# Kernel optimization log

Measured on AMD Instinct MI355X. Metric: run time of the kernel, lower is better.

The kernel has to match this reference:

```python
import jax, jax.numpy as jnp
import numpy as np

B, N, K, H = 8, 256, 64, 768
NUM_CLASSES = 10
D_SIM = 0.3  # self.d in the torch module


def setup_inputs() -> dict:
    key = jax.random.key(0)
    ks = jax.random.split(key, 12)
    s = 0.02  # init scale to keep 3 stacked linear GCN layers numerically tame
    return {
        "encoder_out": jax.random.normal(ks[0], (B, N, H), jnp.float32),
        "landmarks": jax.random.normal(ks[1], (K, H), jnp.float32),
        "alpha": jnp.array([0.5], jnp.float32),
        "gcn_w1": jax.random.normal(ks[2], (H, H), jnp.float32) * s,
        "gcn_b1": jnp.zeros((H,), jnp.float32),
        "gcn_w2": jax.random.normal(ks[3], (H, H), jnp.float32) * s,
        "gcn_b2": jnp.zeros((H,), jnp.float32),
        "gcn_w3": jax.random.normal(ks[4], (H, H), jnp.float32) * s,
        "gcn_b3": jnp.zeros((H,), jnp.float32),
        "fc1_w": jax.random.normal(ks[5], (1000, K * H), jnp.float32) * s,
        "fc1_b": jnp.zeros((1000,), jnp.float32),
        "fc2_w": jax.random.normal(ks[6], (100, 1000), jnp.float32) * s,
        "fc2_b": jnp.zeros((100,), jnp.float32),
        "fc3_w": jax.random.normal(ks[7], (NUM_CLASSES, 100), jnp.float32) * s,
        "fc3_b": jnp.zeros((NUM_CLASSES,), jnp.float32),
    }


def reference(encoder_out, landmarks, alpha,
              gcn_w1, gcn_b1, gcn_w2, gcn_b2, gcn_w3, gcn_b3,
              fc1_w, fc1_b, fc2_w, fc2_b, fc3_w, fc3_b):
    b, n, h = encoder_out.shape
    k = landmarks.shape[0]

    # distance_matrix: [B,N,K], min-max normalized over clusters
    diff = encoder_out[:, :, None, :] - landmarks[None, None, :, :]  # [B,N,K,H]
    dist = jnp.sqrt(jnp.sum(diff * diff, axis=-1))                   # [B,N,K]
    mn = dist.min(axis=-1, keepdims=True)
    mx = dist.max(axis=-1, keepdims=True)
    nd = (dist - mn) / (mx - mn + 1e-6)

    # probability_matrix: gaussian similarity, row-normalized
    sim = jnp.exp(-nd * nd / (2.0 * D_SIM * D_SIM))
    prob = sim / sim.sum(axis=-1, keepdims=True)  # [B,N,K]

    # compute_distance_weight: [N,N] smooth matrix
    idx = jnp.arange(n)
    dw = jnp.exp(-alpha[0] * jnp.abs(idx[:, None] - idx[None, :]).astype(jnp.float32))

    # graph_constructing: einsum('bik,bjl->bijkl') * W then sum over (k,l)
    # == bilinear form P @ W @ P^T, computed WITHOUT the 5-D tensor
    P = prob.transpose(0, 2, 1)                      # [B,K,N]
    G = jnp.einsum('bik,kl,bjl->bij', P, dw, P)      # [B,K,K]

    # cluster pooling: prob^T @ encoder_out -> [B,K,H]
    out = jnp.einsum('bnk,bnh->bkh', prob, encoder_out)
    out_ori = out  # dropout is identity at inference

    # gcn_batched: PyG GCNConv x3 on the dense graph G!=0, batched.
    # gcn_norm: add remaining self-loops, A_hat = A + I_missing,
    # out = D^-1/2 A_hat D^-1/2 (X W^T) + bias  (no nonlinearity between layers)
    A = (G != 0).astype(jnp.float32)                 # [B,K,K]
    A = jnp.maximum(A, jnp.eye(k, dtype=jnp.float32))
    deg = A.sum(axis=-1)                             # [B,K]
    dinv = jnp.where(deg > 0, 1.0 / jnp.sqrt(deg), 0.0)
    An = A * dinv[:, :, None] * dinv[:, None, :]     # normalized adjacency

    hx = out
    for w, bias in ((gcn_w1, gcn_b1), (gcn_w2, gcn_b2), (gcn_w3, gcn_b3)):
        hx = jnp.einsum('bij,bjh->bih', An, hx @ w.T) + bias
    gcn_out = hx + out  # residual inside gcn_batched

    x = (out_ori + gcn_out).reshape(b, -1)           # [B, K*H]
    x = jax.nn.gelu(x @ fc1_w.T + fc1_b, approximate=False)
    x = jax.nn.gelu(x @ fc2_w.T + fc2_b, approximate=False)
    return x @ fc3_w.T + fc3_b                       # [B, NUM_CLASSES]
```

## Files before the change

kernel.cpp:

```cpp
#include <hip/hip_runtime.h>
#include <math.h>

#define DEV __device__ __forceinline__

DEV float dot4(float4 a, float4 b){ return a.x*b.x + a.y*b.y + a.z*b.z + a.w*b.w; }

DEV float wave_sum(float v){
  #pragma unroll
  for (int off = 32; off; off >>= 1) v += __shfl_xor(v, off, 64);
  return v;
}

DEV float gelu_exact(float v){ return 0.5f * v * (1.f + erff(v * 0.70710678118654752f)); }

__global__ void __launch_bounds__(256) k_prob(const float* __restrict__ lm,
                                              const float* __restrict__ enc,
                                              float* __restrict__ prob,
                                              float* __restrict__ y1zero){
  int t = threadIdx.x, lane = t & 63, wv = t >> 6;
  int gid = blockIdx.x*256 + t;
  if (gid < 8000) y1zero[gid] = 0.f;
  int row0 = blockIdx.x*8 + wv*2;
  __shared__ float4 ls[3072];
  const float4* L4 = (const float4*)lm;
  const float4* X0 = (const float4*)(enc + (size_t)row0*768);
  const float4* X1 = X0 + 192;
  float dot0=0.f, dot1=0.f, xn0=0.f, xn1=0.f, ln=0.f;
  for (int c = 0; c < 4; ++c){
    if (c) __syncthreads();
    #pragma unroll
    for (int i = 0; i < 12; ++i){
      int idx = i*256 + t;
      int k = idx & 63, col = idx >> 6;
      ls[idx] = L4[k*192 + c*48 + col];
    }
    __syncthreads();
    #pragma unroll 8
    for (int hg = 0; hg < 48; ++hg){
      float4 l4 = ls[hg*64 + lane];
      float4 a = X0[c*48 + hg], b = X1[c*48 + hg];
      dot0 += dot4(a, l4); dot1 += dot4(b, l4);
      xn0  += dot4(a, a);  xn1  += dot4(b, b);
      ln   += dot4(l4, l4);
    }
  }
  float d0 = sqrtf(fmaxf(xn0 + ln - 2.f*dot0, 0.f));
  float d1 = sqrtf(fmaxf(xn1 + ln - 2.f*dot1, 0.f));
  float mn0=d0, mx0=d0, mn1=d1, mx1=d1;
  #pragma unroll
  for (int off = 32; off; off >>= 1){
    mn0 = fminf(mn0, __shfl_xor(mn0, off, 64));
    mx0 = fmaxf(mx0, __shfl_xor(mx0, off, 64));
    mn1 = fminf(mn1, __shfl_xor(mn1, off, 64));
    mx1 = fmaxf(mx1, __shfl_xor(mx1, off, 64));
  }
  float nd0 = (d0 - mn0) / (mx0 - mn0 + 1e-6f);
  float nd1 = (d1 - mn1) / (mx1 - mn1 + 1e-6f);
  float s0 = expf(nd0*nd0 * (-1.f/0.18f));
  float s1 = expf(nd1*nd1 * (-1.f/0.18f));
  float sum0 = wave_sum(s0), sum1 = wave_sum(s1);
  prob[(size_t)row0*64 + lane]     = s0 / sum0;
  prob[(size_t)(row0+1)*64 + lane] = s1 / sum1;
}

__global__ void k_pool(const float* __restrict__ enc, const float* __restrict__ prob,
                       float* __restrict__ outp, float* __restrict__ mbar){
  int b = blockIdx.x / 48, ch = blockIdx.x % 48;
  int lane = threadIdx.x & 63, wv = threadIdx.x >> 6;
  int h0 = ch*16 + wv*4;
  const float* E = enc + (size_t)b*256*768 + h0;
  const float* P = prob + (size_t)b*256*64;
  float acc[4] = {0,0,0,0};
  #pragma unroll 4
  for (int n = 0; n < 256; ++n){
    float p = P[n*64 + lane];
    float4 e0 = *(const float4*)(E + (size_t)n*768);
    acc[0] += p*e0.x; acc[1] += p*e0.y; acc[2] += p*e0.z; acc[3] += p*e0.w;
  }
  float* O = outp + ((size_t)b*64 + lane)*768 + h0;
  *(float4*)O = make_float4(acc[0],acc[1],acc[2],acc[3]);
  #pragma unroll
  for (int j = 0; j < 4; ++j){
    float v = wave_sum(acc[j]);
    if (lane == 0) mbar[(size_t)b*768 + h0 + j] = v * (1.f/64.f);
  }
}

__global__ void k_vm768(const float* __restrict__ in, const float* __restrict__ W,
                        const float* __restrict__ bias, float* __restrict__ out){
  int lane = threadIdx.x & 63, wv = threadIdx.x >> 6;
  int j = blockIdx.x*4 + wv;
  const float4* Wr = (const float4*)(W + (size_t)j*768);
  const float4* IN = (const float4*)in;
  float acc[8] = {0,0,0,0,0,0,0,0};
  #pragma unroll
  for (int s = 0; s < 3; ++s){
    int ig = s*64 + lane;
    float4 w4 = Wr[ig];
    #pragma unroll
    for (int b = 0; b < 8; ++b) acc[b] += dot4(w4, IN[b*192 + ig]);
  }
  #pragma unroll
  for (int b = 0; b < 8; ++b){
    float v = wave_sum(acc[b]);
    if (lane == 0) out[b*768 + j] = v + bias[j];
  }
}

__global__ void __launch_bounds__(256) k_fc1s(const float* __restrict__ outp,
                                              const float* __restrict__ hx3,
                                              const float* __restrict__ W,
                                              float* __restrict__ y1){
  int t = threadIdx.x, lane = t & 63, wv = t >> 6;
  int kc = blockIdx.x / 125, jg = blockIdx.x % 125;
  int j0 = jg*8;
  const float4* O4 = (const float4*)outp + kc*384;
  const float4* H4 = (const float4*)hx3;
  const float4* Wa = (const float4*)W + (size_t)(j0 + wv*2)*12288 + kc*384;
  const float4* Wb = Wa + 12288;
  __shared__ float4 xs4[3072];
  __shared__ float sp[64];

  float4 wa[6], wb[6];
  #pragma unroll
  for (int s = 0; s < 6; ++s){ wa[s] = Wa[s*64 + lane]; wb[s] = Wb[s*64 + lane]; }

  #pragma unroll
  for (int i = 0; i < 12; ++i){
    int idx = i*256 + t;
    int b = idx / 384, r = idx - b*384;
    int hf4 = r - (r >= 192 ? 192 : 0);
    float4 o = O4[(size_t)b*12288 + r];
    float4 g = H4[b*192 + hf4];
    float4 v;
    v.x = 2.f*o.x + g.x; v.y = 2.f*o.y + g.y; v.z = 2.f*o.z + g.z; v.w = 2.f*o.w + g.w;
    xs4[idx] = v;
  }
  __syncthreads();

  float acc0[8] = {0,0,0,0,0,0,0,0};
  float acc1[8] = {0,0,0,0,0,0,0,0};
  #pragma unroll
  for (int s = 0; s < 6; ++s){
    int ig = s*64 + lane;
    #pragma unroll
    for (int b = 0; b < 8; ++b){
      float4 xv = xs4[b*384 + ig];
      acc0[b] += dot4(wa[s], xv);
      acc1[b] += dot4(wb[s], xv);
    }
  }

  #pragma unroll
  for (int b = 0; b < 8; ++b){
    float v0 = wave_sum(acc0[b]);
    float v1 = wave_sum(acc1[b]);
    if (lane == 0){ sp[(wv*2+0)*8 + b] = v0; sp[(wv*2+1)*8 + b] = v1; }
  }
  __syncthreads();
  if (t < 64){
    int jp = t >> 3, b = t & 7;
    atomicAdd(&y1[b*1000 + j0 + jp], sp[t]);
  }
}

__global__ void __launch_bounds__(256) k_tail(const float* __restrict__ y1,
                                              const float* __restrict__ fb1,
                                              const float* __restrict__ W2,
                                              const float* __restrict__ fb2,
                                              const float* __restrict__ W3,
                                              const float* __restrict__ fb3,
                                              float* __restrict__ out){
  int b = blockIdx.x, t = threadIdx.x, lane = t & 63, wv = t >> 6;
  __shared__ __align__(16) float x1s[1000];
  __shared__ float x2s[100];
  #pragma unroll
  for (int i = 0; i < 4; ++i){
    int j = i*256 + t;
    if (j < 1000) x1s[j] = gelu_exact(y1[b*1000 + j] + fb1[j]);
  }
  __syncthreads();
  const float4* X4 = (const float4*)x1s;
  for (int i = 0; i < 25; ++i){
    int m = wv*25 + i;
    const float4* Wr = (const float4*)(W2 + (size_t)m*1000);
    float acc = 0.f;
    #pragma unroll
    for (int s = 0; s < 4; ++s){
      int jg = s*64 + lane;
      if (jg < 250) acc += dot4(Wr[jg], X4[jg]);
    }
    acc = wave_sum(acc);
    if (lane == 0) x2s[m] = gelu_exact(acc + fb2[m]);
  }
  __syncthreads();
  if (t < 10){
    float acc = fb3[t];
    const float* Wr = W3 + t*100;
    #pragma unroll 4
    for (int m = 0; m < 100; ++m) acc += x2s[m]*Wr[m];
    out[b*10 + t] = acc;
  }
}

extern "C" void kernel_launch(void* const* d_in, const int* in_sizes, int n_in,
                              void* d_out, int out_size, void* d_ws, size_t ws_size,
                              hipStream_t stream){
  const float* enc = (const float*)d_in[0];
  const float* lm  = (const float*)d_in[1];
  const float* w1  = (const float*)d_in[3];
  const float* b1  = (const float*)d_in[4];
  const float* w2  = (const float*)d_in[5];
  const float* b2  = (const float*)d_in[6];
  const float* w3  = (const float*)d_in[7];
  const float* b3  = (const float*)d_in[8];
  const float* fw1 = (const float*)d_in[9];
  const float* fb1 = (const float*)d_in[10];
  const float* fw2 = (const float*)d_in[11];
  const float* fb2 = (const float*)d_in[12];
  const float* fw3 = (const float*)d_in[13];
  const float* fb3 = (const float*)d_in[14];

  float* ws    = (float*)d_ws;
  float* prob  = ws;
  float* outp  = prob  + 131072;
  float* mbar  = outp  + 393216;
  float* hx1   = mbar  + 6144;
  float* hx2   = hx1   + 6144;
  float* hx3   = hx2   + 6144;
  float* y1raw = hx3   + 6144;
  float* out   = (float*)d_out;

  k_prob <<<256, 256, 0, stream>>>(lm, enc, prob, y1raw);
  k_pool <<<384, 256, 0, stream>>>(enc, prob, outp, mbar);
  k_vm768<<<192, 256, 0, stream>>>(mbar, w1, b1, hx1);
  k_vm768<<<192, 256, 0, stream>>>(hx1,  w2, b2, hx2);
  k_vm768<<<192, 256, 0, stream>>>(hx2,  w3, b3, hx3);
  k_fc1s <<<4000,256, 0, stream>>>(outp, hx3, fw1, y1raw);
  k_tail <<<8,   256, 0, stream>>>(y1raw, fb1, fw2, fb2, fw3, fb3, out);
}
```

Measured before the change: 159.2 us.

## Restructure fc1 split-K: 4 rows per wave, partial buffers instead of atomics

The fc1 kernel now gives each wave 4 output rows instead of 2, halving the block count. It reads the activation directly from global/L2 instead of staging it through shared memory, which removes the block barriers. Per-chunk partial sums go to a [32,1000,8] buffer that the tail kernel reduces, replacing the atomicAdd path and the zeroing in k_prob. The trade-offs are more registers per thread (24 float4 weights plus 32 accumulators), repeated global reads of the activation, and a 32-way serial reduction in the tail.

```diff
diff --git a/kernel.cpp b/kernel.cpp
--- a/kernel.cpp
+++ b/kernel.cpp
@@ -15,11 +15,8 @@
 
 __global__ void __launch_bounds__(256) k_prob(const float* __restrict__ lm,
                                               const float* __restrict__ enc,
-                                              float* __restrict__ prob,
-                                              float* __restrict__ y1zero){
+                                              float* __restrict__ prob){
   int t = threadIdx.x, lane = t & 63, wv = t >> 6;
-  int gid = blockIdx.x*256 + t;
-  if (gid < 8000) y1zero[gid] = 0.f;
   int row0 = blockIdx.x*8 + wv*2;
   __shared__ float4 ls[3072];
   const float4* L4 = (const float4*)lm;
@@ -110,61 +107,59 @@
 __global__ void __launch_bounds__(256) k_fc1s(const float* __restrict__ outp,
                                               const float* __restrict__ hx3,
                                               const float* __restrict__ W,
-                                              float* __restrict__ y1){
+                                              float* __restrict__ part){
   int t = threadIdx.x, lane = t & 63, wv = t >> 6;
-  int kc = blockIdx.x / 125, jg = blockIdx.x % 125;
-  int j0 = jg*8;
+  int kc = blockIdx.x / 63, jg = blockIdx.x % 63;
+  int j0 = jg*16 + wv*4;
+  if (j0 >= 1000) return;
   const float4* O4 = (const float4*)outp + kc*384;
   const float4* H4 = (const float4*)hx3;
-  const float4* Wa = (const float4*)W + (size_t)(j0 + wv*2)*12288 + kc*384;
-  const float4* Wb = Wa + 12288;
-  __shared__ float4 xs4[3072];
-  __shared__ float sp[64];
-
-  float4 wa[6], wb[6];
-  #pragma unroll
-  for (int s = 0; s < 6; ++s){ wa[s] = Wa[s*64 + lane]; wb[s] = Wb[s*64 + lane]; }
-
-  #pragma unroll
-  for (int i = 0; i < 12; ++i){
-    int idx = i*256 + t;
-    int b = idx / 384, r = idx - b*384;
-    int hf4 = r - (r >= 192 ? 192 : 0);
-    float4 o = O4[(size_t)b*12288 + r];
-    float4 g = H4[b*192 + hf4];
-    float4 v;
-    v.x = 2.f*o.x + g.x; v.y = 2.f*o.y + g.y; v.z = 2.f*o.z + g.z; v.w = 2.f*o.w + g.w;
-    xs4[idx] = v;
-  }
-  __syncthreads();
-
-  float acc0[8] = {0,0,0,0,0,0,0,0};
-  float acc1[8] = {0,0,0,0,0,0,0,0};
+  const float4* W0 = (const float4*)W + (size_t)j0*12288 + kc*384;
+
+  float4 w[4][6];
+  #pragma unroll
+  for (int r = 0; r < 4; ++r)
+    #pragma unroll
+    for (int s = 0; s < 6; ++s)
+      w[r][s] = W0[(size_t)r*12288 + s*64 + lane];
+
+  float acc[4][8];
+  #pragma unroll
+  for (int r = 0; r < 4; ++r)
+    #pragma unroll
+    for (int b = 0; b < 8; ++b) acc[r][b] = 0.f;
+
   #pragma unroll
   for (int s = 0; s < 6; ++s){
     int ig = s*64 + lane;
+    int hm = ig - (ig >= 192 ? 192 : 0);
     #pragma unroll
     for (int b = 0; b < 8; ++b){
-      float4 xv = xs4[b*384 + ig];
-      acc0[b] += dot4(wa[s], xv);
-      acc1[b] += dot4(wb[s], xv);
-    }
-  }
-
-  #pragma unroll
-  for (int b = 0; b < 8; ++b){
-    float v0 = wave_sum(acc0[b]);
-    float v1 = wave_sum(acc1[b]);
-    if (lane == 0){ sp[(wv*2+0)*8 + b] = v0; sp[(wv*2+1)*8 + b] = v1; }
-  }
-  __syncthreads();
-  if (t < 64){
-    int jp = t >> 3, b = t & 7;
-    atomicAdd(&y1[b*1000 + j0 + jp], sp[t]);
-  }
-}
-
-__global__ void __launch_bounds__(256) k_tail(const float* __restrict__ y1,
+      float4 o = O4[(size_t)b*12288 + ig];
+      float4 g = H4[b*192 + hm];
+      float4 xv;
+      xv.x = 2.f*o.x + g.x; xv.y = 2.f*o.y + g.y;
+      xv.z = 2.f*o.z + g.z; xv.w = 2.f*o.w + g.w;
+      acc[0][b] += dot4(w[0][s], xv);
+      acc[1][b] += dot4(w[1][s], xv);
+      acc[2][b] += dot4(w[2][s], xv);
+      acc[3][b] += dot4(w[3][s], xv);
+    }
+  }
+
+  float v = 0.f;
+  #pragma unroll
+  for (int r = 0; r < 4; ++r)
+    #pragma unroll
+    for (int b = 0; b < 8; ++b){
+      float s = wave_sum(acc[r][b]);
+      v = (lane == r*8 + b) ? s : v;
+    }
+  if (lane < 32)
+    part[(size_t)kc*8000 + (size_t)j0*8 + lane] = v;
+}
+
+__global__ void __launch_bounds__(256) k_tail(const float* __restrict__ part,
                                               const float* __restrict__ fb1,
                                               const float* __restrict__ W2,
                                               const float* __restrict__ fb2,
@@ -177,7 +172,13 @@
   #pragma unroll
   for (int i = 0; i < 4; ++i){
     int j = i*256 + t;
-    if (j < 1000) x1s[j] = gelu_exact(y1[b*1000 + j] + fb1[j]);
+    if (j < 1000){
+      float v = fb1[j];
+      #pragma unroll
+      for (int kc = 0; kc < 32; ++kc)
+        v += part[(size_t)kc*8000 + j*8 + b];
+      x1s[j] = gelu_exact(v);
+    }
   }
   __syncthreads();
   const float4* X4 = (const float4*)x1s;
@@ -228,14 +229,14 @@
   float* hx1   = mbar  + 6144;
   float* hx2   = hx1   + 6144;
   float* hx3   = hx2   + 6144;
-  float* y1raw = hx3   + 6144;
+  float* part  = hx3   + 6144;
   float* out   = (float*)d_out;
 
-  k_prob <<<256, 256, 0, stream>>>(lm, enc, prob, y1raw);
+  k_prob <<<256, 256, 0, stream>>>(lm, enc, prob);
   k_pool <<<384, 256, 0, stream>>>(enc, prob, outp, mbar);
   k_vm768<<<192, 256, 0, stream>>>(mbar, w1, b1, hx1);
   k_vm768<<<192, 256, 0, stream>>>(hx1,  w2, b2, hx2);
   k_vm768<<<192, 256, 0, stream>>>(hx2,  w3, b3, hx3);
-  k_fc1s <<<4000,256, 0, stream>>>(outp, hx3, fw1, y1raw);
-  k_tail <<<8,   256, 0, stream>>>(y1raw, fb1, fw2, fb2, fw3, fb3, out);
-}
+  k_fc1s <<<2016,256, 0, stream>>>(outp, hx3, fw1, part);
+  k_tail <<<8,   256, 0, stream>>>(part, fb1, fw2, fb2, fw3, fb3, out);
+}
```

After: 189.1 us. +18.8%, slower.

## Pipeline fc1 weight loads via direct-to-LDS loads and replace atomics with partial sums

Applied to the files above, without the earlier changes.

A new kernel precomputes the concatenated fc1 input (2*out + gcn residual) into a workspace buffer. The fc1 kernel then streams both inputs and weights into LDS with global_load_lds and a triple-buffered, waitcnt-controlled pipeline. Atomic accumulation into y1 is replaced by per-chunk partial outputs that the tail kernel reduces, so k_prob no longer has to zero y1. This aims to hide weight-load latency and remove atomic contention. The cost is an extra kernel launch and extra workspace traffic for xcat and the partial sums.

```diff
diff --git a/kernel.cpp b/kernel.cpp
--- a/kernel.cpp
+++ b/kernel.cpp
@@ -13,13 +13,15 @@
 
 DEV float gelu_exact(float v){ return 0.5f * v * (1.f + erff(v * 0.70710678118654752f)); }
 
+#define GL16(gsrc, ldst)                                                        \
+  __builtin_amdgcn_global_load_lds(                                             \
+      (const __attribute__((address_space(1))) void*)(gsrc),                    \
+      (__attribute__((address_space(3))) void*)(ldst), 16, 0, 0)
+
 __global__ void __launch_bounds__(256) k_prob(const float* __restrict__ lm,
                                               const float* __restrict__ enc,
-                                              float* __restrict__ prob,
-                                              float* __restrict__ y1zero){
+                                              float* __restrict__ prob){
   int t = threadIdx.x, lane = t & 63, wv = t >> 6;
-  int gid = blockIdx.x*256 + t;
-  if (gid < 8000) y1zero[gid] = 0.f;
   int row0 = blockIdx.x*8 + wv*2;
   __shared__ float4 ls[3072];
   const float4* L4 = (const float4*)lm;
@@ -107,64 +109,85 @@
   }
 }
 
-__global__ void __launch_bounds__(256) k_fc1s(const float* __restrict__ outp,
-                                              const float* __restrict__ hx3,
+__global__ void k_xcat(const float* __restrict__ outp, const float* __restrict__ hx3,
+                       float* __restrict__ x){
+  int idx = blockIdx.x*256 + threadIdx.x;
+  int h4 = idx % 192;
+  int b  = idx / (192*64);
+  float4 o = ((const float4*)outp)[idx];
+  float4 g = ((const float4*)hx3)[b*192 + h4];
+  float4 r;
+  r.x = 2.f*o.x + g.x; r.y = 2.f*o.y + g.y; r.z = 2.f*o.z + g.z; r.w = 2.f*o.w + g.w;
+  ((float4*)x)[idx] = r;
+}
+
+__global__ void __launch_bounds__(256) k_fc1s(const float* __restrict__ xcat,
                                               const float* __restrict__ W,
-                                              float* __restrict__ y1){
+                                              float* __restrict__ part){
   int t = threadIdx.x, lane = t & 63, wv = t >> 6;
   int kc = blockIdx.x / 125, jg = blockIdx.x % 125;
   int j0 = jg*8;
-  const float4* O4 = (const float4*)outp + kc*384;
-  const float4* H4 = (const float4*)hx3;
-  const float4* Wa = (const float4*)W + (size_t)(j0 + wv*2)*12288 + kc*384;
-  const float4* Wb = Wa + 12288;
   __shared__ float4 xs4[3072];
+  __shared__ float4 wb4[1536];
   __shared__ float sp[64];
-
-  float4 wa[6], wb[6];
-  #pragma unroll
-  for (int s = 0; s < 6; ++s){ wa[s] = Wa[s*64 + lane]; wb[s] = Wb[s*64 + lane]; }
-
-  #pragma unroll
-  for (int i = 0; i < 12; ++i){
-    int idx = i*256 + t;
-    int b = idx / 384, r = idx - b*384;
-    int hf4 = r - (r >= 192 ? 192 : 0);
-    float4 o = O4[(size_t)b*12288 + r];
-    float4 g = H4[b*192 + hf4];
-    float4 v;
-    v.x = 2.f*o.x + g.x; v.y = 2.f*o.y + g.y; v.z = 2.f*o.z + g.z; v.w = 2.f*o.w + g.w;
-    xs4[idx] = v;
-  }
+  int rA = 2*wv, rB = 2*wv + 1;
+  const float4* X4 = (const float4*)xcat + kc*384 + lane;
+  const float4* WA = (const float4*)W + (size_t)(j0 + rA)*12288 + kc*384 + lane;
+  const float4* WB = (const float4*)W + (size_t)(j0 + rB)*12288 + kc*384 + lane;
+
+  #pragma unroll
+  for (int q = 0; q < 6; ++q){
+    GL16(X4 + (size_t)rA*12288 + q*64, &xs4[rA*384 + q*64]);
+    GL16(X4 + (size_t)rB*12288 + q*64, &xs4[rB*384 + q*64]);
+  }
+  GL16(WA + 0*64, &wb4[0*512 + rA*64]);
+  GL16(WB + 0*64, &wb4[0*512 + rB*64]);
+  GL16(WA + 1*64, &wb4[1*512 + rA*64]);
+  GL16(WB + 1*64, &wb4[1*512 + rB*64]);
+
+  asm volatile("s_waitcnt vmcnt(4)" ::: "memory");
   __syncthreads();
 
   float acc0[8] = {0,0,0,0,0,0,0,0};
   float acc1[8] = {0,0,0,0,0,0,0,0};
-  #pragma unroll
-  for (int s = 0; s < 6; ++s){
-    int ig = s*64 + lane;
-    #pragma unroll
-    for (int b = 0; b < 8; ++b){
-      float4 xv = xs4[b*384 + ig];
-      acc0[b] += dot4(wa[s], xv);
-      acc1[b] += dot4(wb[s], xv);
-    }
-  }
+
+#define FC1_PHASE(P, ISSUE, WAITSTR)                                       \
+  {                                                                        \
+    if ((ISSUE) >= 0){                                                     \
+      GL16(WA + (ISSUE)*64, &wb4[((ISSUE)%3)*512 + rA*64]);                \
+      GL16(WB + (ISSUE)*64, &wb4[((ISSUE)%3)*512 + rB*64]);                \
+    }                                                                      \
+    asm volatile(WAITSTR ::: "memory");                                    \
+    float4 wA = wb4[((P)%3)*512 + rA*64 + lane];                           \
+    float4 wB = wb4[((P)%3)*512 + rB*64 + lane];                           \
+    _Pragma("unroll")                                                      \
+    for (int b = 0; b < 8; ++b){                                           \
+      float4 xv = xs4[b*384 + (P)*64 + lane];                              \
+      acc0[b] += dot4(wA, xv);                                             \
+      acc1[b] += dot4(wB, xv);                                             \
+    }                                                                      \
+  }
+
+  FC1_PHASE(0, 2, "s_waitcnt vmcnt(4)")
+  FC1_PHASE(1, 3, "s_waitcnt vmcnt(4)")
+  FC1_PHASE(2, 4, "s_waitcnt vmcnt(4)")
+  FC1_PHASE(3, 5, "s_waitcnt vmcnt(4)")
+  FC1_PHASE(4, -1, "s_waitcnt vmcnt(2)")
+  FC1_PHASE(5, -1, "s_waitcnt vmcnt(0)")
+#undef FC1_PHASE
 
   #pragma unroll
   for (int b = 0; b < 8; ++b){
     float v0 = wave_sum(acc0[b]);
     float v1 = wave_sum(acc1[b]);
-    if (lane == 0){ sp[(wv*2+0)*8 + b] = v0; sp[(wv*2+1)*8 + b] = v1; }
-  }
-  __syncthreads();
-  if (t < 64){
-    int jp = t >> 3, b = t & 7;
-    atomicAdd(&y1[b*1000 + j0 + jp], sp[t]);
-  }
-}
-
-__global__ void __launch_bounds__(256) k_tail(const float* __restrict__ y1,
+    if (lane == 0){ sp[rA*8 + b] = v0; sp[rB*8 + b] = v1; }
+  }
+  __syncthreads();
+  if (t < 64)
+    part[(size_t)kc*8000 + (size_t)j0*8 + t] = sp[t];
+}
+
+__global__ void __launch_bounds__(256) k_tail(const float* __restrict__ part,
                                               const float* __restrict__ fb1,
                                               const float* __restrict__ W2,
                                               const float* __restrict__ fb2,
@@ -177,7 +200,13 @@
   #pragma unroll
   for (int i = 0; i < 4; ++i){
     int j = i*256 + t;
-    if (j < 1000) x1s[j] = gelu_exact(y1[b*1000 + j] + fb1[j]);
+    if (j < 1000){
+      float v = fb1[j];
+      #pragma unroll
+      for (int kc = 0; kc < 32; ++kc)
+        v += part[(size_t)kc*8000 + j*8 + b];
+      x1s[j] = gelu_exact(v);
+    }
   }
   __syncthreads();
   const float4* X4 = (const float4*)x1s;
@@ -228,14 +257,16 @@
   float* hx1   = mbar  + 6144;
   float* hx2   = hx1   + 6144;
   float* hx3   = hx2   + 6144;
-  float* y1raw = hx3   + 6144;
+  float* xcat  = hx3   + 6144;
+  float* part  = xcat  + 393216;
   float* out   = (float*)d_out;
 
-  k_prob <<<256, 256, 0, stream>>>(lm, enc, prob, y1raw);
+  k_prob <<<256, 256, 0, stream>>>(lm, enc, prob);
   k_pool <<<384, 256, 0, stream>>>(enc, prob, outp, mbar);
   k_vm768<<<192, 256, 0, stream>>>(mbar, w1, b1, hx1);
   k_vm768<<<192, 256, 0, stream>>>(hx1,  w2, b2, hx2);
   k_vm768<<<192, 256, 0, stream>>>(hx2,  w3, b3, hx3);
-  k_fc1s <<<4000,256, 0, stream>>>(outp, hx3, fw1, y1raw);
-  k_tail <<<8,   256, 0, stream>>>(y1raw, fb1, fw2, fb2, fw3, fb3, out);
-}
+  k_xcat <<<384, 256, 0, stream>>>(outp, hx3, xcat);
+  k_fc1s <<<4000,256, 0, stream>>>(xcat, fw1, part);
+  k_tail <<<8,   256, 0, stream>>>(part, fb1, fw2, fb2, fw3, fb3, out);
+}
```

After: 178.8 us. 12.3% more time.
